# Kernel tuning notes

Measured on AMD Instinct MI355X. Metric: run time of the kernel, lower is better.

The kernel has to match this reference:

```python
import jax, jax.numpy as jnp
import numpy as np

HIDDEN = 1024
NUM_EXPERTS = 16
TOP_K = 6
EPS = 1e-10


def setup_inputs() -> dict:
    key = jax.random.key(0)
    k1, k2, k3, k4 = jax.random.split(key, 4)
    tokens = jax.random.normal(k1, (4, 2048, HIDDEN), dtype=jnp.float32)
    # torch.nn.Linear(hidden_size, num_experts): weight [E, H], bias [E]
    bound = 1.0 / np.sqrt(HIDDEN)
    router_w = jax.random.uniform(k2, (NUM_EXPERTS, HIDDEN), jnp.float32, -bound, bound)
    router_b = jax.random.uniform(k3, (NUM_EXPERTS,), jnp.float32, -bound, bound)
    # expert_weights = randn(E, H, H) / sqrt(H)
    expert_w = jax.random.normal(k4, (NUM_EXPERTS, HIDDEN, HIDDEN), dtype=jnp.float32) / np.sqrt(HIDDEN)
    return {"tokens": tokens, "router_w": router_w, "router_b": router_b, "expert_w": expert_w}


def reference(tokens, router_w, router_b, expert_w):
    B, S, H = tokens.shape
    E = expert_w.shape[0]
    T = B * S

    # Router: softmax -> top-k -> renormalize top-k probs
    logits = jnp.einsum("bsh,eh->bse", tokens, router_w) + router_b  # [B,S,E]
    probs = jax.nn.softmax(logits, axis=-1)
    top_p, top_i = jax.lax.top_k(probs, TOP_K)                        # [B,S,K]
    top_p = top_p / (jnp.sum(top_p, axis=-1, keepdims=True) + EPS)

    x = tokens.reshape(T, H)
    flat_i = top_i.reshape(T, TOP_K)
    flat_p = top_p.reshape(T, TOP_K)

    # Dense gate matrix [T, E]: scatter of normalized top-k weights.
    # Equivalent to the expand/sort/pad + weighted scatter-add restore.
    gate = jnp.zeros((T, E), dtype=flat_p.dtype)
    gate = gate.at[jnp.arange(T)[:, None], flat_i].add(flat_p)
    acc = jnp.maximum(jnp.sum(gate, axis=-1), EPS)  # weight accumulator (clamp min=1e-10)

    # Grouped GEMM equivalent: per-expert matmul weighted by gate, accumulated.
    out = jnp.zeros_like(x)
    for e in range(E):  # fixed, small structural loop over experts
        out = out + (x @ expert_w[e]) * gate[:, e:e + 1]
    out = (out / acc[:, None]).reshape(B, S, H)

    # 'dummy' gradient-connection term from restore_output_with_triton_and_gradients
    out = out + EPS * jnp.sum(top_p, axis=-1, keepdims=True)
    return out
```

## Files before the change

kernel.cpp:

```cpp
#include <hip/hip_runtime.h>
#include <cstdint>
#include <cstddef>

#define NE 16
#define TOPK 6
#define HID 1024
#define NTOK 8192
#define EPSF 1e-10f
#define CAP_ROWS 51200
#define MAXBLK 400

typedef short bf16x8 __attribute__((ext_vector_type(8)));
typedef float f32x4 __attribute__((ext_vector_type(4)));

__device__ __forceinline__ unsigned int f2bf_rne(float f) {
  union { float f; unsigned int u; } v;
  v.f = f;
  return (v.u + 0x7FFFu + ((v.u >> 16) & 1u)) >> 16;
}

__device__ __forceinline__ float bfbits2f(unsigned int hi16) {
  union { unsigned int u; float f; } v;
  v.u = hi16 << 16;
  return v.f;
}

__device__ __forceinline__ void load_lds16(const void* g, void* l) {
  __builtin_amdgcn_global_load_lds(
      (const __attribute__((address_space(1))) void*)g,
      (__attribute__((address_space(3))) void*)l, 16, 0, 0);
}

__global__ __launch_bounds__(256) void router_sparse_kernel(
    const float* __restrict__ tokens, const float* __restrict__ rw,
    const float* __restrict__ rb, unsigned short* __restrict__ Xb,
    unsigned int* __restrict__ topk, float* __restrict__ g6,
    float* __restrict__ epst) {
  __shared__ float s_rw[NE * HID];
  const int tid = threadIdx.x;
  const int wv = tid >> 6;
  const int lane = tid & 63;
  const int token = blockIdx.x * 4 + wv;

  for (int i = tid; i < NE * HID / 4; i += 256)
    ((float4*)s_rw)[i] = ((const float4*)rw)[i];
  __syncthreads();

  const float* xp = tokens + (size_t)token * HID;
  float x[16];
#pragma unroll
  for (int j = 0; j < 16; ++j) x[j] = xp[lane + 64 * j];

  unsigned short* xbrow = Xb + (size_t)token * HID;
#pragma unroll
  for (int j = 0; j < 16; ++j)
    xbrow[lane + 64 * j] = (unsigned short)f2bf_rne(x[j]);

  float lg[NE];
#pragma unroll
  for (int e = 0; e < NE; ++e) {
    const float* w = s_rw + e * HID;
    float p = 0.f;
#pragma unroll
    for (int j = 0; j < 16; ++j) p += x[j] * w[lane + 64 * j];
    lg[e] = p;
  }
#pragma unroll
  for (int m = 1; m < 64; m <<= 1) {
#pragma unroll
    for (int e = 0; e < NE; ++e) lg[e] += __shfl_xor(lg[e], m);
  }
  float mx = -1e30f;
#pragma unroll
  for (int e = 0; e < NE; ++e) {
    lg[e] += rb[e];
    mx = fmaxf(mx, lg[e]);
  }
  float q[NE];
  float s_all = 0.f;
#pragma unroll
  for (int e = 0; e < NE; ++e) {
    q[e] = expf(lg[e] - mx);
    s_all += q[e];
  }
  unsigned sel = 0, pack = 0;
  float s_top = 0.f;
  float gq[TOPK];
#pragma unroll
  for (int k = 0; k < TOPK; ++k) {
    float best = -1.f;
    int bi = 0;
#pragma unroll
    for (int e = 0; e < NE; ++e) {
      bool taken = (sel >> e) & 1u;
      if (!taken && q[e] > best) { best = q[e]; bi = e; }
    }
    sel |= 1u << bi;
    gq[k] = best;
    s_top += best;
    pack |= ((unsigned)bi) << (4 * k);
  }
  if (lane < TOPK)
    g6[(size_t)token * TOPK + lane] = gq[lane] / s_top;
  if (lane == 32) {
    topk[token] = pack;
    float s = s_top / s_all;
    epst[token] = EPSF * (s / (s + EPSF));
  }
}

__global__ __launch_bounds__(256) void sortassign_kernel(
    const unsigned int* __restrict__ topk, const float* __restrict__ g6,
    unsigned int* __restrict__ tokmap, float* __restrict__ gpos,
    unsigned int* __restrict__ inv, unsigned int* __restrict__ table,
    unsigned int* __restrict__ total) {
  __shared__ unsigned int hist[NE];
  __shared__ unsigned int s_seg[NE];
  __shared__ unsigned int s_sc[256];
  const int e = blockIdx.x;
  const int tid = threadIdx.x;

  if (tid < NE) hist[tid] = 0;
  __syncthreads();
  for (int t = tid; t < NTOK; t += 256) {
    const unsigned p = topk[t];
#pragma unroll
    for (int k = 0; k < TOPK; ++k) atomicAdd(&hist[(p >> (4 * k)) & 15u], 1u);
  }
  __syncthreads();
  if (tid == 0) {
    unsigned off = 0;
    for (int i = 0; i < NE; ++i) {
      s_seg[i] = off;
      off += ((hist[i] + 127) >> 7) << 7;
    }
  }
  __syncthreads();
  if (e == 0 && tid == 0) {
    unsigned b = 0;
    for (int i = 0; i < NE; ++i) {
      unsigned mb = (hist[i] + 127) >> 7;
      for (unsigned m = 0; m < mb; ++m)
        table[b++] = ((unsigned)i << 24) | (s_seg[i] + m * 128);
    }
    *total = b;
  }

  const int tbase = tid * (NTOK / 256);
  unsigned c = 0;
  for (int i = 0; i < NTOK / 256; ++i) {
    const unsigned p = topk[tbase + i];
#pragma unroll
    for (int k = 0; k < TOPK; ++k) c += (((p >> (4 * k)) & 15u) == (unsigned)e);
  }
  s_sc[tid] = c;
  __syncthreads();
  for (int off = 1; off < 256; off <<= 1) {
    unsigned v = (tid >= off) ? s_sc[tid - off] : 0u;
    __syncthreads();
    s_sc[tid] += v;
    __syncthreads();
  }
  const unsigned seg0 = s_seg[e];
  unsigned pos = seg0 + s_sc[tid] - c;
  for (int i = 0; i < NTOK / 256; ++i) {
    const int t = tbase + i;
    const unsigned p = topk[t];
#pragma unroll
    for (int k = 0; k < TOPK; ++k) {
      if (((p >> (4 * k)) & 15u) == (unsigned)e) {
        tokmap[pos] = (unsigned)t;
        gpos[pos] = g6[(size_t)t * TOPK + k];
        inv[(size_t)t * TOPK + k] = pos;
        ++pos;
      }
    }
  }
  const unsigned cnt_e = s_sc[255];
  const unsigned segend = seg0 + (((cnt_e + 127) >> 7) << 7);
  for (unsigned p2 = seg0 + cnt_e + tid; p2 < segend; p2 += 256) {
    tokmap[p2] = 0u;
    gpos[p2] = 0.f;
  }
}

__global__ __launch_bounds__(256) void cvt_wt_kernel(
    const float* __restrict__ w, unsigned short* __restrict__ wt) {
  __shared__ float tile[64][65];
  const int kt = blockIdx.x * 64;
  const int nt = blockIdx.y * 64;
  const int e = blockIdx.z;
  const int tr = threadIdx.x >> 6;
  const int tc = threadIdx.x & 63;
  const float* wp = w + (size_t)e * HID * HID;
#pragma unroll
  for (int r = 0; r < 64; r += 4)
    tile[r + tr][tc] = wp[(size_t)(kt + r + tr) * HID + nt + tc];
  __syncthreads();
  unsigned short* wo = wt + (size_t)e * HID * HID;
  const int a = threadIdx.x & 31;
  const int rg = threadIdx.x >> 5;
#pragma unroll
  for (int c = 0; c < 64; c += 8) {
    const int n = c + rg;
    const unsigned lo = f2bf_rne(tile[2 * a][n]);
    const unsigned hi = f2bf_rne(tile[2 * a + 1][n]);
    *(unsigned int*)(wo + (size_t)(nt + n) * HID + kt + 2 * a) = lo | (hi << 16);
  }
}

__global__ __launch_bounds__(256, 4) void moe_ggemm_kernel(
    const unsigned short* __restrict__ Xb, const unsigned short* __restrict__ Wt,
    const unsigned int* __restrict__ table, const unsigned int* __restrict__ total,
    const unsigned int* __restrict__ tokmap, const float* __restrict__ gpos,
    unsigned short* __restrict__ Y) {
  __shared__ unsigned short As[128 * 32];
  __shared__ unsigned short Bs[128 * 32];
  __shared__ unsigned int Ts[128];
  __shared__ float Gs[128];

  const unsigned tot = *total;
  const unsigned bx = blockIdx.x;
  const unsigned slot = bx >> 3;
  if (slot >= tot) return;
  const int n0 = (bx & 7) * 128;
  const unsigned ent = table[slot];
  const int e = ent >> 24;
  const int row0 = ent & 0xFFFFFF;

  const int tid = threadIdx.x;
  const int wv = tid >> 6;
  const int lane = tid & 63;
  const int lm = lane & 15;
  const int quad = lane >> 4;
  const int woff_m = (wv & 1) * 64;
  const int woff_n = (wv >> 1) * 64;

  if (tid < 128) {
    Ts[tid] = tokmap[row0 + tid];
    Gs[tid] = gpos[row0 + tid];
  }
  __syncthreads();

  const int srow = wv * 32 + (lane >> 2);
  const int schunk = (lane & 3) * 16;
  const char* gA0 = (const char*)Xb + (size_t)Ts[srow] * (HID * 2) + schunk;
  const char* gA1 = (const char*)Xb + (size_t)Ts[srow + 16] * (HID * 2) + schunk;
  const char* gB0 = (const char*)Wt + (size_t)e * (HID * HID * 2) +
                    (size_t)(n0 + srow) * (HID * 2) + schunk;
  const char* gB1 = gB0 + 16 * HID * 2;
  char* const lA0 = (char*)As + (wv * 32) * 64;
  char* const lA1 = lA0 + 16 * 64;
  char* const lB0 = (char*)Bs + (wv * 32) * 64;
  char* const lB1 = lB0 + 16 * 64;

  f32x4 acc[4][4];
#pragma unroll
  for (int i = 0; i < 4; ++i)
#pragma unroll
    for (int j = 0; j < 4; ++j) acc[i][j] = (f32x4){0.f, 0.f, 0.f, 0.f};

  for (int ks = 0; ks < 32; ++ks) {
    __syncthreads();
    load_lds16(gA0, lA0);
    load_lds16(gA1, lA1);
    load_lds16(gB0, lB0);
    load_lds16(gB1, lB1);
    gA0 += 64; gA1 += 64; gB0 += 64; gB1 += 64;
    __syncthreads();

    bf16x8 a[4], b[4];
#pragma unroll
    for (int i = 0; i < 4; ++i)
      a[i] = *(const bf16x8*)((const char*)As +
                              (woff_m + 16 * i + lm) * 64 + quad * 16);
#pragma unroll
    for (int j = 0; j < 4; ++j)
      b[j] = *(const bf16x8*)((const char*)Bs +
                              (woff_n + 16 * j + lm) * 64 + quad * 16);
#pragma unroll
    for (int i = 0; i < 4; ++i)
#pragma unroll
      for (int j = 0; j < 4; ++j)
        acc[i][j] =
            __builtin_amdgcn_mfma_f32_16x16x32_bf16(a[i], b[j], acc[i][j], 0, 0, 0);
  }

#pragma unroll
  for (int i = 0; i < 4; ++i)
#pragma unroll
    for (int r = 0; r < 4; ++r) {
      const int row = woff_m + 16 * i + quad * 4 + r;
      const float g = Gs[row];
      unsigned short* yrow = Y + (size_t)(row0 + row) * HID + n0;
#pragma unroll
      for (int j = 0; j < 4; ++j)
        yrow[woff_n + 16 * j + lm] = (unsigned short)f2bf_rne(g * acc[i][j][r]);
    }
}

__global__ __launch_bounds__(256) void reduce_kernel(
    const unsigned short* __restrict__ Y, const unsigned int* __restrict__ inv,
    const float* __restrict__ epst, float* __restrict__ out) {
  const int sub = threadIdx.x >> 7;
  const int ct = threadIdx.x & 127;
  const int t = blockIdx.x * 2 + sub;
  const int c0 = ct * 8;

  float s[8];
  const float ep = epst[t];
#pragma unroll
  for (int i = 0; i < 8; ++i) s[i] = ep;

#pragma unroll
  for (int k = 0; k < TOPK; ++k) {
    const unsigned pos = inv[(size_t)t * TOPK + k];
    const uint4 v = *(const uint4*)(Y + (size_t)pos * HID + c0);
    s[0] += bfbits2f(v.x & 0xFFFFu);
    s[1] += bfbits2f(v.x >> 16);
    s[2] += bfbits2f(v.y & 0xFFFFu);
    s[3] += bfbits2f(v.y >> 16);
    s[4] += bfbits2f(v.z & 0xFFFFu);
    s[5] += bfbits2f(v.z >> 16);
    s[6] += bfbits2f(v.w & 0xFFFFu);
    s[7] += bfbits2f(v.w >> 16);
  }
  float* orow = out + (size_t)t * HID + c0;
  *(float4*)orow = (float4){s[0], s[1], s[2], s[3]};
  *(float4*)(orow + 4) = (float4){s[4], s[5], s[6], s[7]};
}

extern "C" void kernel_launch(void* const* d_in, const int* in_sizes, int n_in,
                              void* d_out, int out_size, void* d_ws, size_t ws_size,
                              hipStream_t stream) {
  const float* tokens = (const float*)d_in[0];
  const float* rw = (const float*)d_in[1];
  const float* rb = (const float*)d_in[2];
  const float* ew = (const float*)d_in[3];
  float* out = (float*)d_out;

  char* ws = (char*)d_ws;
  const size_t OFF_XB = 0;
  const size_t OFF_WT = 16777216;
  const size_t OFF_Y = 50331648;
  const size_t OFF_META = 155189248;
  const size_t M_TOKMAP = OFF_META + 0;
  const size_t M_GPOS = OFF_META + 204800;
  const size_t M_TOTAL = OFF_META + 409600;
  const size_t M_TABLE = OFF_META + 409664;
  const size_t M_INV = OFF_META + 411328;
  const size_t M_TOPK = OFF_META + 607936;
  const size_t M_G6 = OFF_META + 640704;
  const size_t M_EPST = OFF_META + 837312;

  unsigned short* Xb = (unsigned short*)(ws + OFF_XB);
  unsigned short* Wt = (unsigned short*)(ws + OFF_WT);
  unsigned short* Y = (unsigned short*)(ws + OFF_Y);
  unsigned int* tokmap = (unsigned int*)(ws + M_TOKMAP);
  float* gpos = (float*)(ws + M_GPOS);
  unsigned int* total = (unsigned int*)(ws + M_TOTAL);
  unsigned int* table = (unsigned int*)(ws + M_TABLE);
  unsigned int* inv = (unsigned int*)(ws + M_INV);
  unsigned int* topk = (unsigned int*)(ws + M_TOPK);
  float* g6 = (float*)(ws + M_G6);
  float* epst = (float*)(ws + M_EPST);

  router_sparse_kernel<<<dim3(NTOK / 4), dim3(256), 0, stream>>>(
      tokens, rw, rb, Xb, topk, g6, epst);
  cvt_wt_kernel<<<dim3(HID / 64, HID / 64, NE), dim3(256), 0, stream>>>(ew, Wt);
  sortassign_kernel<<<dim3(NE), dim3(256), 0, stream>>>(
      topk, g6, tokmap, gpos, inv, table, total);
  moe_ggemm_kernel<<<dim3(MAXBLK * 8), dim3(256), 0, stream>>>(
      Xb, Wt, table, total, tokmap, gpos, Y);
  reduce_kernel<<<dim3(NTOK / 2), dim3(256), 0, stream>>>(Y, inv, epst, out);
}
```

Baseline: 398.3 us.

## Rewrite grouped GEMM with 256x256 tiles, double-buffered LDS, and fused prep kernel

Moves the grouped GEMM from 128x128 tiles with 256 threads to 256x256 tiles with 512 threads (8 waves). It double-buffers the K=64 LDS stages with an XOR swizzle, interleaves global-to-LDS loads with MFMA phases, and raises wave priority around the MFMAs. A half-tile flag in the block table covers odd 128-row expert segments, and a block-index remap groups work across N tiles. The weight-conversion and sort/assign kernels are merged into a single launch to cut launch overhead. The larger tiles improve data reuse and latency hiding, but they waste compute on half tiles and the LDS footprint lowers occupancy.

```diff
diff --git a/kernel.cpp b/kernel.cpp
--- a/kernel.cpp
+++ b/kernel.cpp
@@ -8,7 +8,8 @@
 #define NTOK 8192
 #define EPSF 1e-10f
 #define CAP_ROWS 51200
-#define MAXBLK 400
+#define MAXB256 208
+#define NT 16
 
 typedef short bf16x8 __attribute__((ext_vector_type(8)));
 typedef float f32x4 __attribute__((ext_vector_type(4)));
@@ -109,16 +110,45 @@
   }
 }
 
-__global__ __launch_bounds__(256) void sortassign_kernel(
+__global__ __launch_bounds__(256) void prep_kernel(
+    const float* __restrict__ ew, unsigned short* __restrict__ wt,
     const unsigned int* __restrict__ topk, const float* __restrict__ g6,
     unsigned int* __restrict__ tokmap, float* __restrict__ gpos,
     unsigned int* __restrict__ inv, unsigned int* __restrict__ table,
     unsigned int* __restrict__ total) {
+  __shared__ float tile[64][65];
   __shared__ unsigned int hist[NE];
   __shared__ unsigned int s_seg[NE];
   __shared__ unsigned int s_sc[256];
+  const int tid = threadIdx.x;
+
+  if (blockIdx.x >= NE) {
+    const int q = blockIdx.x - NE;
+    const int e2 = q >> 8;
+    const int ntile = ((q >> 4) & 15) * 64;
+    const int ktile = (q & 15) * 64;
+    const int tr = tid >> 6;
+    const int tc = tid & 63;
+    const float* wp = ew + (size_t)e2 * HID * HID;
+#pragma unroll
+    for (int r = 0; r < 64; r += 4)
+      tile[r + tr][tc] = wp[(size_t)(ktile + r + tr) * HID + ntile + tc];
+    __syncthreads();
+    unsigned short* wo = wt + (size_t)e2 * HID * HID;
+    const int aa = tid & 31;
+    const int rg = tid >> 5;
+#pragma unroll
+    for (int c2 = 0; c2 < 64; c2 += 8) {
+      const int n = c2 + rg;
+      const unsigned lo = f2bf_rne(tile[2 * aa][n]);
+      const unsigned hi = f2bf_rne(tile[2 * aa + 1][n]);
+      *(unsigned int*)(wo + (size_t)(ntile + n) * HID + ktile + 2 * aa) =
+          lo | (hi << 16);
+    }
+    return;
+  }
+
   const int e = blockIdx.x;
-  const int tid = threadIdx.x;
 
   if (tid < NE) hist[tid] = 0;
   __syncthreads();
@@ -139,9 +169,13 @@
   if (e == 0 && tid == 0) {
     unsigned b = 0;
     for (int i = 0; i < NE; ++i) {
-      unsigned mb = (hist[i] + 127) >> 7;
-      for (unsigned m = 0; m < mb; ++m)
-        table[b++] = ((unsigned)i << 24) | (s_seg[i] + m * 128);
+      const unsigned nb = (hist[i] + 127) >> 7;
+      const unsigned seg = s_seg[i];
+      unsigned m = 0;
+      for (; m + 2 <= nb; m += 2)
+        table[b++] = ((unsigned)i << 24) | (seg + m * 128);
+      if (m < nb)
+        table[b++] = ((unsigned)i << 24) | (1u << 23) | (seg + m * 128);
     }
     *total = b;
   }
@@ -184,119 +218,190 @@
   }
 }
 
-__global__ __launch_bounds__(256) void cvt_wt_kernel(
-    const float* __restrict__ w, unsigned short* __restrict__ wt) {
-  __shared__ float tile[64][65];
-  const int kt = blockIdx.x * 64;
-  const int nt = blockIdx.y * 64;
-  const int e = blockIdx.z;
-  const int tr = threadIdx.x >> 6;
-  const int tc = threadIdx.x & 63;
-  const float* wp = w + (size_t)e * HID * HID;
-#pragma unroll
-  for (int r = 0; r < 64; r += 4)
-    tile[r + tr][tc] = wp[(size_t)(kt + r + tr) * HID + nt + tc];
-  __syncthreads();
-  unsigned short* wo = wt + (size_t)e * HID * HID;
-  const int a = threadIdx.x & 31;
-  const int rg = threadIdx.x >> 5;
-#pragma unroll
-  for (int c = 0; c < 64; c += 8) {
-    const int n = c + rg;
-    const unsigned lo = f2bf_rne(tile[2 * a][n]);
-    const unsigned hi = f2bf_rne(tile[2 * a + 1][n]);
-    *(unsigned int*)(wo + (size_t)(nt + n) * HID + kt + 2 * a) = lo | (hi << 16);
-  }
-}
-
-__global__ __launch_bounds__(256, 4) void moe_ggemm_kernel(
+__global__ __launch_bounds__(512, 2) void moe_ggemm_kernel(
     const unsigned short* __restrict__ Xb, const unsigned short* __restrict__ Wt,
     const unsigned int* __restrict__ table, const unsigned int* __restrict__ total,
     const unsigned int* __restrict__ tokmap, const float* __restrict__ gpos,
     unsigned short* __restrict__ Y) {
-  __shared__ unsigned short As[128 * 32];
-  __shared__ unsigned short Bs[128 * 32];
-  __shared__ unsigned int Ts[128];
-  __shared__ float Gs[128];
+  __shared__ unsigned short As[2][256][64];
+  __shared__ unsigned short Bs[2][256][64];
+  __shared__ unsigned int Ts[256];
+  __shared__ float Gs[256];
 
   const unsigned tot = *total;
   const unsigned bx = blockIdx.x;
-  const unsigned slot = bx >> 3;
+  const unsigned wg = (bx & 7u) * (MAXB256 * 4u / 8u) + (bx >> 3);
+  const unsigned slot = wg >> 2;
   if (slot >= tot) return;
-  const int n0 = (bx & 7) * 128;
+  const int n0 = (int)(wg & 3u) * 256;
   const unsigned ent = table[slot];
-  const int e = ent >> 24;
-  const int row0 = ent & 0xFFFFFF;
+  const int e = (int)(ent >> 24);
+  const int half = (int)((ent >> 23) & 1u);
+  const int row0 = (int)(ent & 0x7FFFFFu);
 
   const int tid = threadIdx.x;
   const int wv = tid >> 6;
   const int lane = tid & 63;
   const int lm = lane & 15;
   const int quad = lane >> 4;
-  const int woff_m = (wv & 1) * 64;
-  const int woff_n = (wv >> 1) * 64;
-
-  if (tid < 128) {
-    Ts[tid] = tokmap[row0 + tid];
-    Gs[tid] = gpos[row0 + tid];
-  }
-  __syncthreads();
-
-  const int srow = wv * 32 + (lane >> 2);
-  const int schunk = (lane & 3) * 16;
-  const char* gA0 = (const char*)Xb + (size_t)Ts[srow] * (HID * 2) + schunk;
-  const char* gA1 = (const char*)Xb + (size_t)Ts[srow + 16] * (HID * 2) + schunk;
-  const char* gB0 = (const char*)Wt + (size_t)e * (HID * HID * 2) +
-                    (size_t)(n0 + srow) * (HID * 2) + schunk;
-  const char* gB1 = gB0 + 16 * HID * 2;
-  char* const lA0 = (char*)As + (wv * 32) * 64;
-  char* const lA1 = lA0 + 16 * 64;
-  char* const lB0 = (char*)Bs + (wv * 32) * 64;
-  char* const lB1 = lB0 + 16 * 64;
-
-  f32x4 acc[4][4];
-#pragma unroll
-  for (int i = 0; i < 4; ++i)
-#pragma unroll
-    for (int j = 0; j < 4; ++j) acc[i][j] = (f32x4){0.f, 0.f, 0.f, 0.f};
-
-  for (int ks = 0; ks < 32; ++ks) {
-    __syncthreads();
-    load_lds16(gA0, lA0);
-    load_lds16(gA1, lA1);
-    load_lds16(gB0, lB0);
-    load_lds16(gB1, lB1);
-    gA0 += 64; gA1 += 64; gB0 += 64; gB1 += 64;
-    __syncthreads();
-
-    bf16x8 a[4], b[4];
-#pragma unroll
-    for (int i = 0; i < 4; ++i)
-      a[i] = *(const bf16x8*)((const char*)As +
-                              (woff_m + 16 * i + lm) * 64 + quad * 16);
-#pragma unroll
-    for (int j = 0; j < 4; ++j)
-      b[j] = *(const bf16x8*)((const char*)Bs +
-                              (woff_n + 16 * j + lm) * 64 + quad * 16);
-#pragma unroll
-    for (int i = 0; i < 4; ++i)
-#pragma unroll
-      for (int j = 0; j < 4; ++j)
-        acc[i][j] =
-            __builtin_amdgcn_mfma_f32_16x16x32_bf16(a[i], b[j], acc[i][j], 0, 0, 0);
-  }
-
-#pragma unroll
-  for (int i = 0; i < 4; ++i)
-#pragma unroll
-    for (int r = 0; r < 4; ++r) {
-      const int row = woff_m + 16 * i + quad * 4 + r;
-      const float g = Gs[row];
-      unsigned short* yrow = Y + (size_t)(row0 + row) * HID + n0;
-#pragma unroll
-      for (int j = 0; j < 4; ++j)
-        yrow[woff_n + 16 * j + lm] = (unsigned short)f2bf_rne(g * acc[i][j][r]);
-    }
+  const int wvm = wv >> 2;
+  const int woff_m = wvm * 128;
+  const int woff_n = (wv & 3) * 64;
+
+  if (tid < 256) {
+    const int rc = (half && tid >= 128) ? 127 : tid;
+    Ts[tid] = tokmap[row0 + rc];
+    Gs[tid] = (half && tid >= 128) ? 0.f : gpos[row0 + rc];
+  }
+  __syncthreads();
+
+  const int srow = tid >> 3;
+  const int scol = ((tid & 7) ^ (srow & 7)) << 4;
+  const char* pA[4];
+  const char* pB[4];
+#pragma unroll
+  for (int i = 0; i < 4; ++i) {
+    pA[i] = (const char*)Xb + (size_t)Ts[i * 64 + srow] * (HID * 2) + scol;
+    pB[i] = (const char*)Wt + (size_t)e * (HID * HID * 2) +
+            (size_t)(n0 + i * 64 + srow) * (HID * 2) + scol;
+  }
+  char* const Ab = (char*)&As[0][0][0];
+  char* const Bb = (char*)&Bs[0][0][0];
+  const int sdst = wv * 8 * 128;
+
+  load_lds16(pA[0], Ab + 0 * 8192 + sdst);
+  load_lds16(pA[2], Ab + 2 * 8192 + sdst);
+  load_lds16(pB[0], Bb + 0 * 8192 + sdst);
+  load_lds16(pB[1], Bb + 1 * 8192 + sdst);
+  load_lds16(pB[2], Bb + 2 * 8192 + sdst);
+  load_lds16(pB[3], Bb + 3 * 8192 + sdst);
+  load_lds16(pA[1], Ab + 1 * 8192 + sdst);
+  load_lds16(pA[3], Ab + 3 * 8192 + sdst);
+
+  f32x4 acc[8][4];
+#pragma unroll
+  for (int f = 0; f < 8; ++f)
+#pragma unroll
+    for (int g = 0; g < 4; ++g) acc[f][g] = (f32x4){0.f, 0.f, 0.f, 0.f};
+
+  const int rsw = (lm & 7) << 4;
+  const int roff0 = (quad * 16) ^ rsw;
+  const int roff1 = (64 + quad * 16) ^ rsw;
+
+  asm volatile("s_waitcnt vmcnt(2)" ::: "memory");
+  __builtin_amdgcn_s_barrier();
+
+  for (int kt = 0; kt < NT; ++kt) {
+    const int c = kt & 1;
+    const int koff = (kt < NT - 1 ? kt + 1 : kt) * 128;
+    const char* ab = Ab + c * 32768;
+    const char* bb = Bb + c * 32768;
+    char* const ast = Ab + (c ^ 1) * 32768;
+    char* const bst = Bb + (c ^ 1) * 32768;
+
+    bf16x8 a[4][2], b[4][2];
+
+#pragma unroll
+    for (int f = 0; f < 4; ++f) {
+      const char* rp = ab + (woff_m + 16 * f + lm) * 128;
+      a[f][0] = *(const bf16x8*)(rp + roff0);
+      a[f][1] = *(const bf16x8*)(rp + roff1);
+    }
+#pragma unroll
+    for (int g = 0; g < 2; ++g) {
+      const char* rp = bb + (woff_n + 16 * g + lm) * 128;
+      b[g][0] = *(const bf16x8*)(rp + roff0);
+      b[g][1] = *(const bf16x8*)(rp + roff1);
+    }
+    load_lds16(pA[0] + koff, ast + 0 * 8192 + sdst);
+    load_lds16(pA[2] + koff, ast + 2 * 8192 + sdst);
+    __builtin_amdgcn_s_barrier();
+    asm volatile("s_waitcnt lgkmcnt(0)" ::: "memory");
+    __builtin_amdgcn_s_setprio(1);
+#pragma unroll
+    for (int f = 0; f < 4; ++f)
+#pragma unroll
+      for (int g = 0; g < 2; ++g) {
+        acc[f][g] = __builtin_amdgcn_mfma_f32_16x16x32_bf16(a[f][0], b[g][0], acc[f][g], 0, 0, 0);
+        acc[f][g] = __builtin_amdgcn_mfma_f32_16x16x32_bf16(a[f][1], b[g][1], acc[f][g], 0, 0, 0);
+      }
+    __builtin_amdgcn_s_setprio(0);
+    __builtin_amdgcn_s_barrier();
+
+#pragma unroll
+    for (int g = 2; g < 4; ++g) {
+      const char* rp = bb + (woff_n + 16 * g + lm) * 128;
+      b[g][0] = *(const bf16x8*)(rp + roff0);
+      b[g][1] = *(const bf16x8*)(rp + roff1);
+    }
+    load_lds16(pB[0] + koff, bst + 0 * 8192 + sdst);
+    load_lds16(pB[1] + koff, bst + 1 * 8192 + sdst);
+    __builtin_amdgcn_s_barrier();
+    asm volatile("s_waitcnt lgkmcnt(0)" ::: "memory");
+    __builtin_amdgcn_s_setprio(1);
+#pragma unroll
+    for (int f = 0; f < 4; ++f)
+#pragma unroll
+      for (int g = 2; g < 4; ++g) {
+        acc[f][g] = __builtin_amdgcn_mfma_f32_16x16x32_bf16(a[f][0], b[g][0], acc[f][g], 0, 0, 0);
+        acc[f][g] = __builtin_amdgcn_mfma_f32_16x16x32_bf16(a[f][1], b[g][1], acc[f][g], 0, 0, 0);
+      }
+    __builtin_amdgcn_s_setprio(0);
+    asm volatile("s_waitcnt vmcnt(4)" ::: "memory");
+    __builtin_amdgcn_s_barrier();
+
+#pragma unroll
+    for (int f = 0; f < 4; ++f) {
+      const char* rp = ab + (woff_m + 16 * (f + 4) + lm) * 128;
+      a[f][0] = *(const bf16x8*)(rp + roff0);
+      a[f][1] = *(const bf16x8*)(rp + roff1);
+    }
+    load_lds16(pB[2] + koff, bst + 2 * 8192 + sdst);
+    load_lds16(pB[3] + koff, bst + 3 * 8192 + sdst);
+    __builtin_amdgcn_s_barrier();
+    asm volatile("s_waitcnt lgkmcnt(0)" ::: "memory");
+    __builtin_amdgcn_s_setprio(1);
+#pragma unroll
+    for (int f = 0; f < 4; ++f)
+#pragma unroll
+      for (int g = 2; g < 4; ++g) {
+        acc[f + 4][g] = __builtin_amdgcn_mfma_f32_16x16x32_bf16(a[f][0], b[g][0], acc[f + 4][g], 0, 0, 0);
+        acc[f + 4][g] = __builtin_amdgcn_mfma_f32_16x16x32_bf16(a[f][1], b[g][1], acc[f + 4][g], 0, 0, 0);
+      }
+    __builtin_amdgcn_s_setprio(0);
+    __builtin_amdgcn_s_barrier();
+
+    load_lds16(pA[1] + koff, ast + 1 * 8192 + sdst);
+    load_lds16(pA[3] + koff, ast + 3 * 8192 + sdst);
+    __builtin_amdgcn_s_barrier();
+    __builtin_amdgcn_s_setprio(1);
+#pragma unroll
+    for (int f = 0; f < 4; ++f)
+#pragma unroll
+      for (int g = 0; g < 2; ++g) {
+        acc[f + 4][g] = __builtin_amdgcn_mfma_f32_16x16x32_bf16(a[f][0], b[g][0], acc[f + 4][g], 0, 0, 0);
+        acc[f + 4][g] = __builtin_amdgcn_mfma_f32_16x16x32_bf16(a[f][1], b[g][1], acc[f + 4][g], 0, 0, 0);
+      }
+    __builtin_amdgcn_s_setprio(0);
+    asm volatile("s_waitcnt vmcnt(2)" ::: "memory");
+    __builtin_amdgcn_s_barrier();
+  }
+
+  asm volatile("s_waitcnt vmcnt(0)" ::: "memory");
+
+  if (!(half && wvm)) {
+#pragma unroll
+    for (int f = 0; f < 8; ++f)
+#pragma unroll
+      for (int r = 0; r < 4; ++r) {
+        const int row = woff_m + 16 * f + quad * 4 + r;
+        const float gte = Gs[row];
+        unsigned short* yrow = Y + (size_t)(row0 + row) * HID + n0;
+#pragma unroll
+        for (int g = 0; g < 4; ++g)
+          yrow[woff_n + 16 * g + lm] = (unsigned short)f2bf_rne(gte * acc[f][g][r]);
+      }
+  }
 }
 
 __global__ __launch_bounds__(256) void reduce_kernel(
@@ -367,10 +472,9 @@
 
   router_sparse_kernel<<<dim3(NTOK / 4), dim3(256), 0, stream>>>(
       tokens, rw, rb, Xb, topk, g6, epst);
-  cvt_wt_kernel<<<dim3(HID / 64, HID / 64, NE), dim3(256), 0, stream>>>(ew, Wt);
-  sortassign_kernel<<<dim3(NE), dim3(256), 0, stream>>>(
-      topk, g6, tokmap, gpos, inv, table, total);
-  moe_ggemm_kernel<<<dim3(MAXBLK * 8), dim3(256), 0, stream>>>(
+  prep_kernel<<<dim3(NE + (HID / 64) * (HID / 64) * NE), dim3(256), 0, stream>>>(
+      ew, Wt, topk, g6, tokmap, gpos, inv, table, total);
+  moe_ggemm_kernel<<<dim3(MAXB256 * 4), dim3(512), 0, stream>>>(
       Xb, Wt, table, total, tokmap, gpos, Y);
   reduce_kernel<<<dim3(NTOK / 2), dim3(256), 0, stream>>>(Y, inv, epst, out);
 }
```

After: 364.6 us. 8.5% less time.
